# Kernel tuning notes

Hardware: AMD Instinct MI355X
Metric: run time of the kernel (lower is better)

Reference implementation:

```python
import jax, jax.numpy as jnp
import numpy as np
from jax import lax

B, C, H, W, K = 32, 128, 56, 56, 5
CR = C // 4          # reduced channels in weight-gen MLP
CE = 4 * C           # expanded channels
EPS = 1e-6


def setup_inputs() -> dict:
    key = jax.random.key(0)
    ks = jax.random.split(key, 8)
    s = lambda fan: 1.0 / np.sqrt(fan)
    return {
        "x": jax.random.normal(ks[0], (B, C, H, W), jnp.float32),
        "w_fc1": jax.random.normal(ks[1], (CR, C), jnp.float32) * s(C),
        "ln1_w": jnp.ones((CR,), jnp.float32),
        "ln1_b": jnp.zeros((CR,), jnp.float32),
        "w_fc2": jax.random.normal(ks[2], (C * K * K, CR), jnp.float32) * s(CR),
        "ln2_w": jnp.ones((C,), jnp.float32),
        "ln2_b": jnp.zeros((C,), jnp.float32),
        "w_expand": jax.random.normal(ks[3], (CE, C), jnp.float32) * s(C),
        "w_shrink": jax.random.normal(ks[4], (C, CE), jnp.float32) * s(CE),
        "grn_gamma": jax.random.normal(ks[5], (CE,), jnp.float32) * 0.1,
        "grn_beta": jax.random.normal(ks[6], (CE,), jnp.float32) * 0.1,
    }


def _ln(v, w, b, axis):
    u = v.mean(axis, keepdims=True)
    s2 = jnp.square(v - u).mean(axis, keepdims=True)
    return (v - u) * lax.rsqrt(s2 + EPS) * w + b


def reference(x, w_fc1, ln1_w, ln1_b, w_fc2, ln2_w, ln2_b, w_expand, w_shrink,
              grn_gamma, grn_beta):
    b, c, h, w = x.shape
    # ---- dynamic weight generation: pool -> fc1 -> LN -> fc2 ----
    pooled = x.mean((2, 3))                                  # [B, C]
    hdn = pooled @ w_fc1.T                                   # [B, CR]
    hdn = _ln(hdn, ln1_w, ln1_b, axis=-1)                    # channels_first LN over CR
    dyn = hdn @ w_fc2.T                                      # [B, C*K*K]
    dyn_w = dyn.reshape(b * c, 1, K, K)                      # per-sample depthwise kernels
    # ---- per-sample dynamic depthwise conv (groups = B*C) ----
    pad = K // 2
    out = lax.conv_general_dilated(
        x.reshape(1, b * c, h, w), dyn_w,
        window_strides=(1, 1), padding=[(pad, pad), (pad, pad)],
        dimension_numbers=("NCHW", "OIHW", "NCHW"),
        feature_group_count=b * c,
    ).reshape(b, c, h, w)
    # ---- LN (channels_first) over channel dim ----
    u = out.mean(1, keepdims=True)
    s2 = jnp.square(out - u).mean(1, keepdims=True)
    out = (out - u) * lax.rsqrt(s2 + EPS)
    out = ln2_w[None, :, None, None] * out + ln2_b[None, :, None, None]
    # ---- expand 1x1 -> GELU -> GRN -> shrink 1x1 ----
    out = jnp.einsum("bchw,oc->bohw", out, w_expand)         # [B, 4C, H, W]
    out = jax.nn.gelu(out, approximate=False)
    gx = jnp.sqrt(jnp.sum(jnp.square(out), axis=(2, 3), keepdims=True))  # [B,4C,1,1]
    nx = gx / (gx.mean(1, keepdims=True) + EPS)
    g = grn_gamma[None, :, None, None]
    bt = grn_beta[None, :, None, None]
    out = g * (out * nx) + bt + out
    out = jnp.einsum("bohw,co->bchw", out, w_shrink)         # [B, C, H, W]
    return out + x
```

## Files before the change

### kernel.cpp

```cpp
#include <hip/hip_runtime.h>
#include <hip/hip_bf16.h>

#define B_   32
#define C_   128
#define H_   56
#define W_   56
#define HW_  (H_*W_)
#define BHW_ (B_*HW_)
#define K5_  5
#define KK_  25
#define CR_  32
#define CE_  512
#define EPS_ 1e-6f

typedef __hip_bfloat16 bf16;
typedef __attribute__((ext_vector_type(8))) short short8;
typedef __attribute__((ext_vector_type(4))) float f32x4;


__device__ __forceinline__ float wave_reduce_sum(float v) {
#pragma unroll
  for (int off = 32; off > 0; off >>= 1) v += __shfl_down(v, off, 64);
  return v;
}
__device__ __forceinline__ float bf2f(unsigned short u) {
  return __uint_as_float(((unsigned)u) << 16);
}
__device__ __forceinline__ unsigned short f2bf_bits(float f) {
  bf16 h = __float2bfloat16(f);
  unsigned short u;
  __builtin_memcpy(&u, &h, 2);
  return u;
}
__device__ __forceinline__ float fast_gelu(float v) {
  float t = __expf(-1.702f * v);
  return v * __builtin_amdgcn_rcpf(1.0f + t);
}
__device__ __forceinline__ void glds16(const void* g, void* l) {
  __builtin_amdgcn_global_load_lds(
      (const __attribute__((address_space(1))) unsigned int*)g,
      (__attribute__((address_space(3))) unsigned int*)l, 16, 0, 0);
}

__global__ __launch_bounds__(256) void prep_kernel(const float* __restrict__ we,
                                                   const float* __restrict__ ws,
                                                   bf16* __restrict__ weB,
                                                   bf16* __restrict__ wsB,
                                                   float* __restrict__ gx2) {
  int i = blockIdx.x * 256 + threadIdx.x;
  if (i < CE_ * C_)          weB[i] = __float2bfloat16(we[i]);
  else if (i < 2 * CE_ * C_) wsB[i - CE_ * C_] = __float2bfloat16(ws[i - CE_ * C_]);
  else                       gx2[i - 2 * CE_ * C_] = 0.f;
}

__global__ __launch_bounds__(256) void pool_kernel(const float* __restrict__ x,
                                                   float* __restrict__ pooled) {
  int bc = blockIdx.x;
  const float4* xp4 = reinterpret_cast<const float4*>(x + (size_t)bc * HW_);
  float s = 0.f;
  for (int i = threadIdx.x; i < 784; i += 256) {
    float4 v = xp4[i];
    s += (v.x + v.y) + (v.z + v.w);
  }
  s = wave_reduce_sum(s);
  __shared__ float red[4];
  int lane = threadIdx.x & 63, wid = threadIdx.x >> 6;
  if (lane == 0) red[wid] = s;
  __syncthreads();
  if (threadIdx.x == 0) pooled[bc] = (red[0] + red[1] + red[2] + red[3]) * (1.0f / HW_);
}

__global__ __launch_bounds__(256) void fc_kernel(const float* __restrict__ pooled,
                                                 const float* __restrict__ w_fc1,
                                                 const float* __restrict__ ln1_w,
                                                 const float* __restrict__ ln1_b,
                                                 const float* __restrict__ w_fc2,
                                                 float* __restrict__ dyn) {
  int b = blockIdx.x;
  int tid = threadIdx.x;
  __shared__ float sp[C_];
  __shared__ float sh[CR_];
  __shared__ float shn[CR_];
  __shared__ float stats[2];
  if (tid < C_) sp[tid] = pooled[b * C_ + tid];
  __syncthreads();
  if (tid < CR_) {
    float acc = 0.f;
    const float* wr = w_fc1 + tid * C_;
#pragma unroll 4
    for (int c = 0; c < C_; ++c) acc += sp[c] * wr[c];
    sh[tid] = acc;
  }
  __syncthreads();
  if (tid == 0) {
    float u = 0.f;
    for (int j = 0; j < CR_; ++j) u += sh[j];
    u *= (1.0f / CR_);
    float v = 0.f;
    for (int j = 0; j < CR_; ++j) { float d = sh[j] - u; v += d * d; }
    v *= (1.0f / CR_);
    stats[0] = u;
    stats[1] = rsqrtf(v + EPS_);
  }
  __syncthreads();
  if (tid < CR_) shn[tid] = (sh[tid] - stats[0]) * stats[1] * ln1_w[tid] + ln1_b[tid];
  __syncthreads();
  for (int i = tid; i < C_ * KK_; i += 256) {
    const float* wr = w_fc2 + i * CR_;
    float acc = 0.f;
#pragma unroll
    for (int j = 0; j < CR_; ++j) acc += shn[j] * wr[j];
    dyn[b * (C_ * KK_) + i] = acc;
  }
}

__global__ __launch_bounds__(256) void conv_kernel(const float* __restrict__ x,
                                                   const float* __restrict__ dyn,
                                                   bf16* __restrict__ z) {
  int bc = blockIdx.x;
  int b = bc >> 7;
  int c = bc & 127;
  int tid = threadIdx.x;
  __shared__ float xs[(H_ + 4) * 64];
  __shared__ float wks[KK_];
  {
    int r = tid >> 6;
    int rr = (r < 2) ? r : (56 + r);
    xs[rr * 64 + (tid & 63)] = 0.f;
  }
  if (tid < 224) {
    int r = tid >> 2, q = tid & 3;
    int col = (q < 2) ? q : (56 + q);
    xs[(r + 2) * 64 + col] = 0.f;
  }
  if (tid < KK_) wks[tid] = dyn[b * (C_ * KK_) + c * KK_ + tid];
  const float4* xp4 = reinterpret_cast<const float4*>(x + (size_t)bc * HW_);
  for (int i = tid; i < 784; i += 256) {
    float4 v = xp4[i];
    int h = i / 14, w4 = (i % 14) * 4;
    float* dst = &xs[(h + 2) * 64 + 2 + w4];
    dst[0] = v.x; dst[1] = v.y; dst[2] = v.z; dst[3] = v.w;
  }
  __syncthreads();
  float wr[KK_];
#pragma unroll
  for (int j = 0; j < KK_; ++j) wr[j] = wks[j];
  for (int g = tid; g < 784; g += 256) {
    int h = g / 14;
    int w4 = (g % 14) * 4;
    float a0 = 0.f, a1 = 0.f, a2 = 0.f, a3 = 0.f;
#pragma unroll
    for (int dh = 0; dh < K5_; ++dh) {
      const float* row = &xs[(h + dh) * 64 + w4];
      float4 va = *reinterpret_cast<const float4*>(row);
      float4 vb = *reinterpret_cast<const float4*>(row + 4);
      float v0 = va.x, v1 = va.y, v2 = va.z, v3 = va.w;
      float v4 = vb.x, v5 = vb.y, v6 = vb.z, v7 = vb.w;
      float u0 = wr[dh * 5 + 0], u1 = wr[dh * 5 + 1], u2 = wr[dh * 5 + 2];
      float u3 = wr[dh * 5 + 3], u4 = wr[dh * 5 + 4];
      a0 += v0 * u0 + v1 * u1 + v2 * u2 + v3 * u3 + v4 * u4;
      a1 += v1 * u0 + v2 * u1 + v3 * u2 + v4 * u3 + v5 * u4;
      a2 += v2 * u0 + v3 * u1 + v4 * u2 + v5 * u3 + v6 * u4;
      a3 += v3 * u0 + v4 * u1 + v5 * u2 + v6 * u3 + v7 * u4;
    }
    size_t base = (size_t)bc * HW_ + h * W_ + w4;
    ushort4 pk = make_ushort4(f2bf_bits(a0), f2bf_bits(a1), f2bf_bits(a2), f2bf_bits(a3));
    *reinterpret_cast<ushort4*>(reinterpret_cast<unsigned short*>(z) + base) = pk;
  }
}

__global__ __launch_bounds__(256) void ln_kernel(const bf16* __restrict__ z,
                                                 const float* __restrict__ ln2_w,
                                                 const float* __restrict__ ln2_b,
                                                 bf16* __restrict__ yT) {
  int hw0 = blockIdx.x * 64;
  int b = blockIdx.y;
  int tid = threadIdx.x;
  int wq = tid & 63;
  int cq = tid >> 6;
  __shared__ unsigned short zt[C_][64];
  __shared__ unsigned short yt[64][136];
  __shared__ float redS[4][64];
  __shared__ float redQ[4][64];
  __shared__ float meanArr[64];
  __shared__ float invArr[64];
  const unsigned short* zp = reinterpret_cast<const unsigned short*>(z);
#pragma unroll
  for (int i = 0; i < 4; ++i) {
    int t = tid + 256 * i;
    int c = t >> 3, ch = t & 7;
    int4 v = *reinterpret_cast<const int4*>(zp + ((size_t)(b * C_ + c)) * HW_ + hw0 + ch * 8);
    *reinterpret_cast<int4*>(&zt[c][ch * 8]) = v;
  }
  __syncthreads();
  float s = 0.f, q = 0.f;
#pragma unroll 4
  for (int k = 0; k < 32; ++k) {
    float v = bf2f(zt[cq * 32 + k][wq]);
    s += v;
    q += v * v;
  }
  redS[cq][wq] = s;
  redQ[cq][wq] = q;
  __syncthreads();
  if (cq == 0) {
    float ss = redS[0][wq] + redS[1][wq] + redS[2][wq] + redS[3][wq];
    float qq = redQ[0][wq] + redQ[1][wq] + redQ[2][wq] + redQ[3][wq];
    float m = ss * (1.0f / C_);
    float var = qq * (1.0f / C_) - m * m;
    meanArr[wq] = m;
    invArr[wq] = rsqrtf(fmaxf(var, 0.f) + EPS_);
  }
  __syncthreads();
  float m = meanArr[wq], iv = invArr[wq];
#pragma unroll
  for (int g = 0; g < 4; ++g) {
    unsigned short pk[8];
#pragma unroll
    for (int i = 0; i < 8; ++i) {
      int c = cq * 32 + g * 8 + i;
      float v = bf2f(zt[c][wq]);
      pk[i] = f2bf_bits((v - m) * iv * ln2_w[c] + ln2_b[c]);
    }
    int4 t;
    __builtin_memcpy(&t, pk, 16);
    *reinterpret_cast<int4*>(&yt[wq][cq * 32 + g * 8]) = t;
  }
  __syncthreads();
  unsigned short* yp = reinterpret_cast<unsigned short*>(yT);
#pragma unroll
  for (int i = 0; i < 4; ++i) {
    int t = tid + 256 * i;
    int row = t >> 4, ch = t & 15;
    int4 v = *reinterpret_cast<const int4*>(&yt[row][ch * 8]);
    *reinterpret_cast<int4*>(yp + ((size_t)(b * HW_ + hw0 + row)) * C_ + ch * 8) = v;
  }
}

__global__ __launch_bounds__(256, 4) void expand_mfma(const bf16* __restrict__ yT,
                                                      const bf16* __restrict__ weB,
                                                      bf16* __restrict__ eT,
                                                      float* __restrict__ gx2) {
  int j0 = blockIdx.x * 128;
  int o0 = blockIdx.y * 128;
  int tid = threadIdx.x;
  int lane = tid & 63, wid = tid >> 6;
  int wm = wid >> 1, wn = wid & 1;
  int quad = lane >> 4, l15 = lane & 15;
  __shared__ __align__(16) char smem[34816];
  const short* yS = reinterpret_cast<const short*>(yT);
  const short* weS = reinterpret_cast<const short*>(weB);
  int sr = (wid * 2) * 16 + (lane >> 2);
  int scp = lane & 3;
  auto STAGE = [&](int bs, int k0) {
#pragma unroll
    for (int i = 0; i < 2; ++i) {
      int seg = wid * 2 + i;
      int r = sr + i * 16;
      int c = scp ^ ((r >> 1) & 3);
      char* base = smem + bs * 16384 + seg * 1024;
      glds16(yS + (size_t)(j0 + r) * C_ + k0 + c * 8, base);
      glds16(weS + (size_t)(o0 + r) * C_ + k0 + c * 8, base + 8192);
    }
  };
  f32x4 acc[4][4] = {};
  STAGE(0, 0);
  __syncthreads();
#pragma unroll
  for (int t = 0; t < 4; ++t) {
    if (t < 3) STAGE((t + 1) & 1, (t + 1) * 32);
    const char* ba = smem + (t & 1) * 16384;
    int sx = (quad ^ ((l15 >> 1) & 3)) * 16;
    short8 a[4], bfr[4];
#pragma unroll
    for (int mf = 0; mf < 4; ++mf)
      a[mf] = *reinterpret_cast<const short8*>(ba + (wm * 64 + mf * 16 + l15) * 64 + sx);
#pragma unroll
    for (int nf = 0; nf < 4; ++nf)
      bfr[nf] = *reinterpret_cast<const short8*>(ba + 8192 + (wn * 64 + nf * 16 + l15) * 64 + sx);
#pragma unroll
    for (int mf = 0; mf < 4; ++mf)
#pragma unroll
      for (int nf = 0; nf < 4; ++nf)
        acc[mf][nf] = __builtin_amdgcn_mfma_f32_16x16x32_bf16(a[mf], bfr[nf], acc[mf][nf], 0, 0, 0);
    __syncthreads();
  }
  short (*Es)[136] = reinterpret_cast<short(*)[136]>(&smem[0]);
#pragma unroll
  for (int mf = 0; mf < 4; ++mf) {
    int jm = j0 + wm * 64 + mf * 16;
    int bb = jm / HW_;
    int jrow = wm * 64 + mf * 16 + quad * 4;
#pragma unroll
    for (int nf = 0; nf < 4; ++nf) {
      int oc = wn * 64 + nf * 16 + l15;
      float g2 = 0.f;
#pragma unroll
      for (int r = 0; r < 4; ++r) {
        float ge = fast_gelu(acc[mf][nf][r]);
        g2 += ge * ge;
        Es[jrow + r][oc] = (short)f2bf_bits(ge);
      }
      g2 += __shfl_xor(g2, 16, 64);
      g2 += __shfl_xor(g2, 32, 64);
      if (quad == 0) atomicAdd(&gx2[bb * CE_ + o0 + oc], g2);
    }
  }
  __syncthreads();
  unsigned short* eP = reinterpret_cast<unsigned short*>(eT);
#pragma unroll
  for (int i = 0; i < 8; ++i) {
    int t = tid + 256 * i;
    int row = t >> 4, ch = t & 15;
    int4 v = *reinterpret_cast<const int4*>(&Es[row][ch * 8]);
    *reinterpret_cast<int4*>(eP + (size_t)(j0 + row) * CE_ + o0 + ch * 8) = v;
  }
}

__global__ __launch_bounds__(512) void grn_scale_kernel(const float* __restrict__ gx2,
                                                        const float* __restrict__ gamma,
                                                        float* __restrict__ scale) {
  int b = blockIdx.x;
  int o = threadIdx.x;
  float gx = sqrtf(gx2[b * CE_ + o]);
  float s = wave_reduce_sum(gx);
  __shared__ float red[8];
  __shared__ float meansh;
  int lane = o & 63, wid = o >> 6;
  if (lane == 0) red[wid] = s;
  __syncthreads();
  if (o == 0) {
    float t = 0.f;
    for (int i = 0; i < 8; ++i) t += red[i];
    meansh = t * (1.0f / CE_);
  }
  __syncthreads();
  scale[b * CE_ + o] = 1.0f + gamma[o] * (gx / (meansh + EPS_));
}

__global__ __launch_bounds__(256) void sb_kernel(const float* __restrict__ w_shrink,
                                                 const float* __restrict__ beta,
                                                 float* __restrict__ sb) {
  int c = blockIdx.x;
  const float* wp = w_shrink + (size_t)c * CE_;
  float acc = 0.f;
  for (int o = threadIdx.x; o < CE_; o += 256) acc += wp[o] * beta[o];
  acc = wave_reduce_sum(acc);
  __shared__ float red[4];
  int lane = threadIdx.x & 63, wid = threadIdx.x >> 6;
  if (lane == 0) red[wid] = acc;
  __syncthreads();
  if (threadIdx.x == 0) sb[c] = red[0] + red[1] + red[2] + red[3];
}

__global__ __launch_bounds__(256) void scale_ws_kernel(const float* __restrict__ ws,
                                                       const float* __restrict__ scale,
                                                       bf16* __restrict__ sws) {
  int c = blockIdx.x;
  int b = blockIdx.y;
  const float* sp = scale + b * CE_;
  const float* wp = ws + (size_t)c * CE_;
  bf16* op = sws + ((size_t)(b * C_ + c)) * CE_;
  for (int i = threadIdx.x; i < CE_; i += 256)
    op[i] = __float2bfloat16(wp[i] * sp[i]);
}

__global__ __launch_bounds__(256, 3) void shrink_mfma(const bf16* __restrict__ eT,
                                                      const bf16* __restrict__ sws,
                                                      const float* __restrict__ sb,
                                                      const float* __restrict__ x,
                                                      float* __restrict__ out) {
  int hw0 = blockIdx.x * 64;
  int b = blockIdx.y;
  int tid = threadIdx.x;
  int lane = tid & 63, wid = tid >> 6;
  int wm = wid >> 1, wn = wid & 1;
  int quad = lane >> 4, l15 = lane & 15;
  __shared__ __align__(16) char smem[49152];
  const short* eS  = reinterpret_cast<const short*>(eT) + (size_t)b * HW_ * CE_;
  const short* wsS = reinterpret_cast<const short*>(sws) + (size_t)b * C_ * CE_;
  int lr = lane >> 3;
  int lc = lane & 7;
  auto STAGE = [&](int bs, int k0) {
    char* base = smem + bs * 24576;
#pragma unroll
    for (int i = 0; i < 2; ++i) {
      int seg = wid * 2 + i;
      int r = seg * 8 + lr;
      int c = lc ^ (r & 7);
      glds16(eS + (size_t)(hw0 + r) * CE_ + k0 + c * 8, base + seg * 1024);
    }
#pragma unroll
    for (int i = 0; i < 4; ++i) {
      int seg = wid * 4 + i;
      int r = seg * 8 + lr;
      int c = lc ^ (r & 7);
      glds16(wsS + (size_t)r * CE_ + k0 + c * 8, base + 8192 + seg * 1024);
    }
  };
  f32x4 acc[2][4] = {};
  STAGE(0, 0);
  __syncthreads();
#pragma unroll 1
  for (int t = 0; t < 8; ++t) {
    if (t < 7) STAGE((t + 1) & 1, (t + 1) * 64);
    const char* ba = smem + (t & 1) * 24576;
#pragma unroll
    for (int ks = 0; ks < 2; ++ks) {
      short8 a[2], bfr[4];
#pragma unroll
      for (int mf = 0; mf < 2; ++mf) {
        int row = wm * 32 + mf * 16 + l15;
        int cp = (ks * 4 + quad) ^ (row & 7);
        a[mf] = *reinterpret_cast<const short8*>(ba + row * 128 + cp * 16);
      }
#pragma unroll
      for (int nf = 0; nf < 4; ++nf) {
        int row = wn * 64 + nf * 16 + l15;
        int cp = (ks * 4 + quad) ^ (row & 7);
        bfr[nf] = *reinterpret_cast<const short8*>(ba + 8192 + row * 128 + cp * 16);
      }
#pragma unroll
      for (int mf = 0; mf < 2; ++mf)
#pragma unroll
        for (int nf = 0; nf < 4; ++nf)
          acc[mf][nf] = __builtin_amdgcn_mfma_f32_16x16x32_bf16(a[mf], bfr[nf], acc[mf][nf], 0, 0, 0);
    }
    __syncthreads();
  }
  float (*Ef)[68] = reinterpret_cast<float(*)[68]>(&smem[0]);
#pragma unroll
  for (int mf = 0; mf < 2; ++mf) {
    int hwr = wm * 32 + mf * 16 + quad * 4;
#pragma unroll
    for (int nf = 0; nf < 4; ++nf)
      *reinterpret_cast<f32x4*>(&Ef[wn * 64 + nf * 16 + l15][hwr]) = acc[mf][nf];
  }
  __syncthreads();
#pragma unroll
  for (int i = 0; i < 8; ++i) {
    int t = tid + 256 * i;
    int row = t >> 4, ch = t & 15;
    int hw = hw0 + ch * 4;
    size_t base = ((size_t)(b * C_ + row)) * HW_ + hw;
    float add = sb[row];
    f32x4 av = *reinterpret_cast<const f32x4*>(&Ef[row][ch * 4]);
    float4 xv = *reinterpret_cast<const float4*>(x + base);
    float4 ov;
    ov.x = av.x + add + xv.x;
    ov.y = av.y + add + xv.y;
    ov.z = av.z + add + xv.z;
    ov.w = av.w + add + xv.w;
    *reinterpret_cast<float4*>(out + base) = ov;
  }
}

extern "C" void kernel_launch(void* const* d_in, const int* in_sizes, int n_in,
                              void* d_out, int out_size, void* d_ws, size_t ws_size,
                              hipStream_t stream) {
  (void)in_sizes; (void)n_in; (void)out_size; (void)ws_size;
  const float* x        = (const float*)d_in[0];
  const float* w_fc1    = (const float*)d_in[1];
  const float* ln1_w    = (const float*)d_in[2];
  const float* ln1_b    = (const float*)d_in[3];
  const float* w_fc2    = (const float*)d_in[4];
  const float* ln2_w    = (const float*)d_in[5];
  const float* ln2_b    = (const float*)d_in[6];
  const float* w_expand = (const float*)d_in[7];
  const float* w_shrink = (const float*)d_in[8];
  const float* gamma    = (const float*)d_in[9];
  const float* beta     = (const float*)d_in[10];
  float* out = (float*)d_out;

  char* ws = (char*)d_ws;
  float* pooled = (float*)(ws + 0);
  float* dyn    = (float*)(ws + 16384);
  float* gx2    = (float*)(ws + 425984);
  float* scale  = (float*)(ws + 491520);
  float* sb     = (float*)(ws + 557056);
  bf16*  weB    = (bf16*)(ws + 557568);
  bf16*  wsB    = (bf16*)(ws + 688640);
  bf16*  yT     = (bf16*)(ws + 819712);
  bf16*  sws    = (bf16*)(ws + 819712);
  bf16*  eT     = (bf16*)(ws + 26509824);
  bf16*  z      = eT;

  prep_kernel<<<576, 256, 0, stream>>>(w_expand, w_shrink, weB, wsB, gx2);
  sb_kernel<<<C_, 256, 0, stream>>>(w_shrink, beta, sb);
  pool_kernel<<<B_ * C_, 256, 0, stream>>>(x, pooled);
  fc_kernel<<<B_, 256, 0, stream>>>(pooled, w_fc1, ln1_w, ln1_b, w_fc2, dyn);
  conv_kernel<<<B_ * C_, 256, 0, stream>>>(x, dyn, z);
  ln_kernel<<<dim3(49, B_), 256, 0, stream>>>(z, ln2_w, ln2_b, yT);
  expand_mfma<<<dim3(784, 4), 256, 0, stream>>>(yT, weB, eT, gx2);
  grn_scale_kernel<<<B_, 512, 0, stream>>>(gx2, gamma, scale);
  scale_ws_kernel<<<dim3(C_, B_), 256, 0, stream>>>(w_shrink, scale, sws);
  shrink_mfma<<<dim3(49, B_), 256, 0, stream>>>(eT, sws, sb, x, out);
}
```

Before: 264.3 us.

## Recompute expand GEMM inside shrink kernel instead of materializing expanded activations

The expand pass now only computes the GRN sum-of-squares and no longer writes the bf16 expanded tensor. The shrink kernel recomputes the expand GEMM per 128-channel chunk, applies GELU and the GRN scale, and feeds the result straight into the shrink GEMM from shared memory. This removes the write and re-read of the large [B*HW, 4C] intermediate and the per-sample scaled-weight kernel. The sb computation is also folded into the prep kernel. The cost is doing the expand GEMM twice, plus lower occupancy from the larger shared-memory footprint and no double buffering in the fused kernel.

```diff
diff --git a/kernel.cpp b/kernel.cpp
--- a/kernel.cpp
+++ b/kernel.cpp
@@ -44,13 +44,28 @@
 
 __global__ __launch_bounds__(256) void prep_kernel(const float* __restrict__ we,
                                                    const float* __restrict__ ws,
+                                                   const float* __restrict__ beta,
                                                    bf16* __restrict__ weB,
                                                    bf16* __restrict__ wsB,
-                                                   float* __restrict__ gx2) {
-  int i = blockIdx.x * 256 + threadIdx.x;
-  if (i < CE_ * C_)          weB[i] = __float2bfloat16(we[i]);
-  else if (i < 2 * CE_ * C_) wsB[i - CE_ * C_] = __float2bfloat16(ws[i - CE_ * C_]);
-  else                       gx2[i - 2 * CE_ * C_] = 0.f;
+                                                   float* __restrict__ gx2,
+                                                   float* __restrict__ sb) {
+  if (blockIdx.x < 576) {
+    int i = blockIdx.x * 256 + threadIdx.x;
+    if (i < CE_ * C_)          weB[i] = __float2bfloat16(we[i]);
+    else if (i < 2 * CE_ * C_) wsB[i - CE_ * C_] = __float2bfloat16(ws[i - CE_ * C_]);
+    else                       gx2[i - 2 * CE_ * C_] = 0.f;
+  } else {
+    int c = blockIdx.x - 576;
+    const float* wp = ws + (size_t)c * CE_;
+    float acc = 0.f;
+    for (int o = threadIdx.x; o < CE_; o += 256) acc += wp[o] * beta[o];
+    acc = wave_reduce_sum(acc);
+    __shared__ float red[4];
+    int lane = threadIdx.x & 63, wid = threadIdx.x >> 6;
+    if (lane == 0) red[wid] = acc;
+    __syncthreads();
+    if (threadIdx.x == 0) sb[c] = red[0] + red[1] + red[2] + red[3];
+  }
 }
 
 __global__ __launch_bounds__(256) void pool_kernel(const float* __restrict__ x,
@@ -237,17 +252,16 @@
   }
 }
 
-__global__ __launch_bounds__(256, 4) void expand_mfma(const bf16* __restrict__ yT,
-                                                      const bf16* __restrict__ weB,
-                                                      bf16* __restrict__ eT,
-                                                      float* __restrict__ gx2) {
+__global__ __launch_bounds__(256, 4) void gx2_pass(const bf16* __restrict__ yT,
+                                                   const bf16* __restrict__ weB,
+                                                   float* __restrict__ gx2) {
   int j0 = blockIdx.x * 128;
   int o0 = blockIdx.y * 128;
   int tid = threadIdx.x;
   int lane = tid & 63, wid = tid >> 6;
   int wm = wid >> 1, wn = wid & 1;
   int quad = lane >> 4, l15 = lane & 15;
-  __shared__ __align__(16) char smem[34816];
+  __shared__ __align__(16) char smem[32768];
   const short* yS = reinterpret_cast<const short*>(yT);
   const short* weS = reinterpret_cast<const short*>(weB);
   int sr = (wid * 2) * 16 + (lane >> 2);
@@ -285,35 +299,20 @@
         acc[mf][nf] = __builtin_amdgcn_mfma_f32_16x16x32_bf16(a[mf], bfr[nf], acc[mf][nf], 0, 0, 0);
     __syncthreads();
   }
-  short (*Es)[136] = reinterpret_cast<short(*)[136]>(&smem[0]);
 #pragma unroll
   for (int mf = 0; mf < 4; ++mf) {
     int jm = j0 + wm * 64 + mf * 16;
     int bb = jm / HW_;
-    int jrow = wm * 64 + mf * 16 + quad * 4;
 #pragma unroll
     for (int nf = 0; nf < 4; ++nf) {
       int oc = wn * 64 + nf * 16 + l15;
       float g2 = 0.f;
 #pragma unroll
-      for (int r = 0; r < 4; ++r) {
-        float ge = fast_gelu(acc[mf][nf][r]);
-        g2 += ge * ge;
-        Es[jrow + r][oc] = (short)f2bf_bits(ge);
-      }
+      for (int r = 0; r < 4; ++r) { float ge = fast_gelu(acc[mf][nf][r]); g2 += ge * ge; }
       g2 += __shfl_xor(g2, 16, 64);
       g2 += __shfl_xor(g2, 32, 64);
       if (quad == 0) atomicAdd(&gx2[bb * CE_ + o0 + oc], g2);
     }
-  }
-  __syncthreads();
-  unsigned short* eP = reinterpret_cast<unsigned short*>(eT);
-#pragma unroll
-  for (int i = 0; i < 8; ++i) {
-    int t = tid + 256 * i;
-    int row = t >> 4, ch = t & 15;
-    int4 v = *reinterpret_cast<const int4*>(&Es[row][ch * 8]);
-    *reinterpret_cast<int4*>(eP + (size_t)(j0 + row) * CE_ + o0 + ch * 8) = v;
   }
 }
 
@@ -338,93 +337,109 @@
   scale[b * CE_ + o] = 1.0f + gamma[o] * (gx / (meansh + EPS_));
 }
 
-__global__ __launch_bounds__(256) void sb_kernel(const float* __restrict__ w_shrink,
-                                                 const float* __restrict__ beta,
-                                                 float* __restrict__ sb) {
-  int c = blockIdx.x;
-  const float* wp = w_shrink + (size_t)c * CE_;
-  float acc = 0.f;
-  for (int o = threadIdx.x; o < CE_; o += 256) acc += wp[o] * beta[o];
-  acc = wave_reduce_sum(acc);
-  __shared__ float red[4];
-  int lane = threadIdx.x & 63, wid = threadIdx.x >> 6;
-  if (lane == 0) red[wid] = acc;
-  __syncthreads();
-  if (threadIdx.x == 0) sb[c] = red[0] + red[1] + red[2] + red[3];
-}
-
-__global__ __launch_bounds__(256) void scale_ws_kernel(const float* __restrict__ ws,
+__global__ __launch_bounds__(256, 2) void fused_shrink(const bf16* __restrict__ yT,
+                                                       const bf16* __restrict__ weB,
+                                                       const bf16* __restrict__ wsB,
                                                        const float* __restrict__ scale,
-                                                       bf16* __restrict__ sws) {
-  int c = blockIdx.x;
-  int b = blockIdx.y;
-  const float* sp = scale + b * CE_;
-  const float* wp = ws + (size_t)c * CE_;
-  bf16* op = sws + ((size_t)(b * C_ + c)) * CE_;
-  for (int i = threadIdx.x; i < CE_; i += 256)
-    op[i] = __float2bfloat16(wp[i] * sp[i]);
-}
-
-__global__ __launch_bounds__(256, 3) void shrink_mfma(const bf16* __restrict__ eT,
-                                                      const bf16* __restrict__ sws,
-                                                      const float* __restrict__ sb,
-                                                      const float* __restrict__ x,
-                                                      float* __restrict__ out) {
+                                                       const float* __restrict__ sb,
+                                                       const float* __restrict__ x,
+                                                       float* __restrict__ out) {
   int hw0 = blockIdx.x * 64;
   int b = blockIdx.y;
   int tid = threadIdx.x;
   int lane = tid & 63, wid = tid >> 6;
   int wm = wid >> 1, wn = wid & 1;
   int quad = lane >> 4, l15 = lane & 15;
-  __shared__ __align__(16) char smem[49152];
-  const short* eS  = reinterpret_cast<const short*>(eT) + (size_t)b * HW_ * CE_;
-  const short* wsS = reinterpret_cast<const short*>(sws) + (size_t)b * C_ * CE_;
-  int lr = lane >> 3;
-  int lc = lane & 7;
-  auto STAGE = [&](int bs, int k0) {
-    char* base = smem + bs * 24576;
-#pragma unroll
-    for (int i = 0; i < 2; ++i) {
-      int seg = wid * 2 + i;
-      int r = seg * 8 + lr;
-      int c = lc ^ (r & 7);
-      glds16(eS + (size_t)(hw0 + r) * CE_ + k0 + c * 8, base + seg * 1024);
-    }
-#pragma unroll
-    for (int i = 0; i < 4; ++i) {
-      int seg = wid * 4 + i;
-      int r = seg * 8 + lr;
-      int c = lc ^ (r & 7);
-      glds16(wsS + (size_t)r * CE_ + k0 + c * 8, base + 8192 + seg * 1024);
-    }
-  };
-  f32x4 acc[2][4] = {};
-  STAGE(0, 0);
-  __syncthreads();
+  __shared__ __align__(16) char smem[66048];
+  const short* yS  = reinterpret_cast<const short*>(yT) + (size_t)b * HW_ * C_;
+  const short* weS = reinterpret_cast<const short*>(weB);
+  const short* wsS = reinterpret_cast<const short*>(wsB);
+  const float* scp = scale + b * CE_;
+  short (*Es)[132] = reinterpret_cast<short(*)[132]>(smem + 49152);
+  int lr4 = lane >> 4;
+  int lc16 = lane & 15;
+#pragma unroll
+  for (int i = 0; i < 4; ++i) {
+    int seg = wid * 4 + i;
+    int r = seg * 4 + lr4;
+    int csrc = lc16 ^ (r & 15);
+    glds16(yS + (size_t)(hw0 + r) * C_ + csrc * 8, smem + seg * 1024);
+  }
+  f32x4 acc2[2][4] = {};
 #pragma unroll 1
-  for (int t = 0; t < 8; ++t) {
-    if (t < 7) STAGE((t + 1) & 1, (t + 1) * 64);
-    const char* ba = smem + (t & 1) * 24576;
-#pragma unroll
-    for (int ks = 0; ks < 2; ++ks) {
+  for (int n = 0; n < 4; ++n) {
+    int oc0 = n * 128;
+#pragma unroll
+    for (int i = 0; i < 8; ++i) {
+      int seg = wid * 8 + i;
+      int r = seg * 4 + lr4;
+      int csrc = lc16 ^ (r & 15);
+      glds16(weS + (size_t)(oc0 + r) * C_ + csrc * 8, smem + 16384 + seg * 1024);
+    }
+    __syncthreads();
+    f32x4 acc1[2][4] = {};
+#pragma unroll
+    for (int ks = 0; ks < 4; ++ks) {
       short8 a[2], bfr[4];
 #pragma unroll
       for (int mf = 0; mf < 2; ++mf) {
         int row = wm * 32 + mf * 16 + l15;
-        int cp = (ks * 4 + quad) ^ (row & 7);
-        a[mf] = *reinterpret_cast<const short8*>(ba + row * 128 + cp * 16);
+        int cp = (ks * 4 + quad) ^ (row & 15);
+        a[mf] = *reinterpret_cast<const short8*>(smem + row * 256 + cp * 16);
       }
 #pragma unroll
       for (int nf = 0; nf < 4; ++nf) {
         int row = wn * 64 + nf * 16 + l15;
-        int cp = (ks * 4 + quad) ^ (row & 7);
-        bfr[nf] = *reinterpret_cast<const short8*>(ba + 8192 + row * 128 + cp * 16);
+        int cp = (ks * 4 + quad) ^ (row & 15);
+        bfr[nf] = *reinterpret_cast<const short8*>(smem + 16384 + row * 256 + cp * 16);
       }
 #pragma unroll
       for (int mf = 0; mf < 2; ++mf)
 #pragma unroll
         for (int nf = 0; nf < 4; ++nf)
-          acc[mf][nf] = __builtin_amdgcn_mfma_f32_16x16x32_bf16(a[mf], bfr[nf], acc[mf][nf], 0, 0, 0);
+          acc1[mf][nf] = __builtin_amdgcn_mfma_f32_16x16x32_bf16(a[mf], bfr[nf], acc1[mf][nf], 0, 0, 0);
+    }
+    __syncthreads();
+#pragma unroll
+    for (int nf = 0; nf < 4; ++nf) {
+      int ocl = wn * 64 + nf * 16 + l15;
+      float sc = scp[oc0 + ocl];
+#pragma unroll
+      for (int mf = 0; mf < 2; ++mf) {
+        int jrow = wm * 32 + mf * 16 + quad * 4;
+#pragma unroll
+        for (int r = 0; r < 4; ++r)
+          Es[jrow + r][ocl] = (short)f2bf_bits(fast_gelu(acc1[mf][nf][r]) * sc);
+      }
+    }
+#pragma unroll
+    for (int i = 0; i < 8; ++i) {
+      int seg = wid * 8 + i;
+      int r = seg * 4 + lr4;
+      int csrc = lc16 ^ (r & 15);
+      glds16(wsS + (size_t)r * CE_ + oc0 + csrc * 8, smem + 16384 + seg * 1024);
+    }
+    __syncthreads();
+#pragma unroll
+    for (int ks = 0; ks < 4; ++ks) {
+      short8 a2[2], b2[4];
+#pragma unroll
+      for (int mf = 0; mf < 2; ++mf) {
+        int row = wm * 32 + mf * 16 + l15;
+        a2[mf] = *reinterpret_cast<const short8*>(
+            reinterpret_cast<const char*>(Es) + row * 264 + ks * 64 + quad * 16);
+      }
+#pragma unroll
+      for (int nf = 0; nf < 4; ++nf) {
+        int row = wn * 64 + nf * 16 + l15;
+        int cp = (ks * 4 + quad) ^ (row & 15);
+        b2[nf] = *reinterpret_cast<const short8*>(smem + 16384 + row * 256 + cp * 16);
+      }
+#pragma unroll
+      for (int mf = 0; mf < 2; ++mf)
+#pragma unroll
+        for (int nf = 0; nf < 4; ++nf)
+          acc2[mf][nf] = __builtin_amdgcn_mfma_f32_16x16x32_bf16(a2[mf], b2[nf], acc2[mf][nf], 0, 0, 0);
     }
     __syncthreads();
   }
@@ -434,7 +449,7 @@
     int hwr = wm * 32 + mf * 16 + quad * 4;
 #pragma unroll
     for (int nf = 0; nf < 4; ++nf)
-      *reinterpret_cast<f32x4*>(&Ef[wn * 64 + nf * 16 + l15][hwr]) = acc[mf][nf];
+      *reinterpret_cast<f32x4*>(&Ef[wn * 64 + nf * 16 + l15][hwr]) = acc2[mf][nf];
   }
   __syncthreads();
 #pragma unroll
@@ -481,18 +496,14 @@
   bf16*  weB    = (bf16*)(ws + 557568);
   bf16*  wsB    = (bf16*)(ws + 688640);
   bf16*  yT     = (bf16*)(ws + 819712);
-  bf16*  sws    = (bf16*)(ws + 819712);
-  bf16*  eT     = (bf16*)(ws + 26509824);
-  bf16*  z      = eT;
-
-  prep_kernel<<<576, 256, 0, stream>>>(w_expand, w_shrink, weB, wsB, gx2);
-  sb_kernel<<<C_, 256, 0, stream>>>(w_shrink, beta, sb);
+  bf16*  z      = (bf16*)(ws + 26509824);
+
+  prep_kernel<<<704, 256, 0, stream>>>(w_expand, w_shrink, beta, weB, wsB, gx2, sb);
   pool_kernel<<<B_ * C_, 256, 0, stream>>>(x, pooled);
   fc_kernel<<<B_, 256, 0, stream>>>(pooled, w_fc1, ln1_w, ln1_b, w_fc2, dyn);
   conv_kernel<<<B_ * C_, 256, 0, stream>>>(x, dyn, z);
   ln_kernel<<<dim3(49, B_), 256, 0, stream>>>(z, ln2_w, ln2_b, yT);
-  expand_mfma<<<dim3(784, 4), 256, 0, stream>>>(yT, weB, eT, gx2);
+  gx2_pass<<<dim3(784, 4), 256, 0, stream>>>(yT, weB, gx2);
   grn_scale_kernel<<<B_, 512, 0, stream>>>(gx2, gamma, scale);
-  scale_ws_kernel<<<dim3(C_, B_), 256, 0, stream>>>(w_shrink, scale, sws);
-  shrink_mfma<<<dim3(49, B_), 256, 0, stream>>>(eT, sws, sb, x, out);
-}
+  fused_shrink<<<dim3(49, B_), 256, 0, stream>>>(yT, weB, wsB, scale, sb, x, out);
+}
```

After: 278.4 us. 1.05x slower.
